# Optimization experiments

Hardware: AMD Instinct MI355X
Metric: run time of the kernel (lower is better)

Reference implementation:

```python
import jax, jax.numpy as jnp
import numpy as np

C = 64          # channels
L = 2           # GRU layers
DEC_STEPS = 35


def setup_inputs() -> dict:
    key = jax.random.key(0)
    ks = jax.random.split(key, 10)
    B, S = 2048, 512
    s = 0.1  # small init scale keeps gates in linear-ish region
    return {
        "pulse":    jax.random.normal(ks[0], (B, S, 2), dtype=jnp.float32),
        "dense1_w": jax.random.normal(ks[1], (C, 2), dtype=jnp.float32) * s,
        "dense1_b": jax.random.normal(ks[2], (C,), dtype=jnp.float32) * s,
        "dense2_w": jax.random.normal(ks[3], (2, C), dtype=jnp.float32) * s,
        "dense2_b": jax.random.normal(ks[4], (2,), dtype=jnp.float32) * s,
        "Wih":      jax.random.normal(ks[5], (L, 3 * C, C), dtype=jnp.float32) * s,
        "Whh":      jax.random.normal(ks[6], (L, 3 * C, C), dtype=jnp.float32) * s,
        "bih":      jax.random.normal(ks[7], (L, 3 * C), dtype=jnp.float32) * s,
        "bhh":      jax.random.normal(ks[8], (L, 3 * C), dtype=jnp.float32) * s,
        "embed":    jax.random.normal(ks[9], (1, C), dtype=jnp.float32) * s,
    }


def _gru_cell(x, h, wih, whh, bi, bh):
    # PyTorch GRU cell math (gate order r, z, n)
    gi = x @ wih.T + bi   # [B, 3C]
    gh = h @ whh.T + bh   # [B, 3C]
    ir, iz, inn = jnp.split(gi, 3, axis=-1)
    hr, hz, hn = jnp.split(gh, 3, axis=-1)
    r = jax.nn.sigmoid(ir + hr)
    z = jax.nn.sigmoid(iz + hz)
    n = jnp.tanh(inn + r * hn)
    return (1.0 - z) * n + z * h


def _multi_step(h_stack, x, Wih, Whh, bih, bhh):
    # One timestep through L stacked GRU layers. h_stack: [L, B, C]
    new_h = []
    inp = x
    for l in range(L):
        hl = _gru_cell(inp, h_stack[l], Wih[l], Whh[l], bih[l], bhh[l])
        new_h.append(hl)
        inp = hl
    return jnp.stack(new_h), inp  # (new state stack, top-layer output)


def reference(pulse, dense1_w, dense1_b, dense2_w, dense2_b, Wih, Whh, bih, bhh, embed):
    B = pulse.shape[0]
    # dense1 then time-major [S, B, C]
    x = pulse @ dense1_w.T + dense1_b
    x = jnp.transpose(x, (1, 0, 2))
    h0 = jnp.zeros((L, B, C), dtype=x.dtype)

    def enc_step(h, xt):
        h2, _ = _multi_step(h, xt, Wih, Whh, bih, bhh)
        return h2, None

    hT, _ = jax.lax.scan(enc_step, h0, x)  # encoder final state [L, B, C]

    sos = jnp.broadcast_to(embed[0], (B, C))  # embedding of token 0

    def dec_step(carry, _):
        latest, h = carry
        h2, out = _multi_step(h, latest, Wih, Whh, bih, bhh)
        return (out, h2), out

    _, outs = jax.lax.scan(dec_step, (sos, hT), None, length=DEC_STEPS)  # [35, B, C]

    # dense2 on decoder outputs; slicing pred[:, 1:, :] in the source drops the
    # sos position, which equals applying dense2 to the 35 decoder outputs only.
    pred = jnp.transpose(outs, (1, 0, 2)) @ dense2_w.T + dense2_b  # [B, 35, 2]
    return pred
```

## Files before the change

kernel.cpp:

```cpp
#include <hip/hip_runtime.h>
#include <math.h>


#define CCH  64
#define GG   192
#define SEQ  512
#define DECS 35
#define BT   8
#define NTH  512
#define NW   8
#define STG_SH (16 * 17 * 8)

typedef __attribute__((ext_vector_type(8))) short bf16x8;
typedef __attribute__((ext_vector_type(4))) float f32x4;

__device__ __forceinline__ short f2b(float f) {
  union { float f; unsigned u; } v; v.f = f;
  unsigned r = v.u + 0x7fffu + ((v.u >> 16) & 1u);
  return (short)(r >> 16);
}
__device__ __forceinline__ float sigf(float x) { return 1.0f / (1.0f + __expf(-x)); }
__device__ __forceinline__ float tanhfast(float x) {
  float t = __expf(-2.0f * fabsf(x));
  float r = (1.0f - t) / (1.0f + t);
  return copysignf(r, x);
}
__device__ __forceinline__ int stoff(int col, int k) {
  return ((k >> 3) * 17 + col) * 8 + (k & 7);
}

extern "C" __global__ void __launch_bounds__(NTH, 2)
gru_lane(const float* __restrict__ pulse,
         const float* __restrict__ d1w,
         const float* __restrict__ d1b,
         const float* __restrict__ d2w,
         const float* __restrict__ d2b,
         const float* __restrict__ Wih,
         const float* __restrict__ Whh,
         const float* __restrict__ bih,
         const float* __restrict__ bhh,
         const float* __restrict__ embed,
         float* __restrict__ out)
{
  __shared__ __align__(16) unsigned short stA[STG_SH];
  __shared__ __align__(16) unsigned short stC[STG_SH];
  __shared__ float red[NW * 16];

  const int tid = threadIdx.x;
  const int wid = tid >> 6;
  const int l   = tid & 63;
  const int lm  = l & 15;
  const int lg  = l >> 4;
  const int b   = lm & 7;
  const int ch  = wid * 8 + ((lm >> 3) << 2) + lg;
  const int bgb = blockIdx.x * BT;

  for (int i = tid; i < STG_SH; i += NTH) { stA[i] = 0; stC[i] = 0; }

  const float* Wih0 = Wih;
  const float* Whh0 = Whh;
  const float* Wih1 = Wih + GG * CCH;
  const float* Whh1 = Whh + GG * CCH;
  const int sub = lm & 3;
  bf16x8 bA[2][4], bC[2][4];
#pragma unroll
  for (int t = 0; t < 2; ++t) {
    const int wch = wid * 8 + t * 4 + (lm >> 2);
    const int rr  = (sub == 0 ? wch : (sub == 1 ? 64 + wch : 128 + wch));
#pragma unroll
    for (int s = 0; s < 4; ++s) {
#pragma unroll
      for (int e = 0; e < 8; ++e) {
        int kk = 32 * s + 8 * lg + e;
        float va, vc;
        if (sub == 2) {
          va = kk < 64 ? Wih0[rr * CCH + kk] : 0.f;
          vc = kk < 64 ? Wih1[rr * CCH + kk] : 0.f;
        } else if (sub == 3) {
          va = kk < 64 ? 0.f : Whh0[rr * CCH + kk - 64];
          vc = kk < 64 ? 0.f : Whh1[rr * CCH + kk - 64];
        } else {
          va = kk < 64 ? Wih0[rr * CCH + kk] : Whh0[rr * CCH + kk - 64];
          vc = kk < 64 ? Wih1[rr * CCH + kk] : Whh1[rr * CCH + kk - 64];
        }
        bA[t][s][e] = f2b(va);
        bC[t][s][e] = f2b(vc);
      }
    }
  }

  float A0f[3], A1f[3], C0f[3];
#pragma unroll
  for (int g = 0; g < 3; ++g) {
    int row = g * CCH + ch;
    float a0 = 0.f, a1 = 0.f, cc = 0.f;
    for (int k = 0; k < CCH; ++k) {
      float wv = Wih0[row * CCH + k];
      a0 += wv * d1w[2 * k];
      a1 += wv * d1w[2 * k + 1];
      cc += wv * d1b[k];
    }
    A0f[g] = a0; A1f[g] = a1; C0f[g] = cc + bih[row];
  }
  const float bh0r = bhh[ch], bh0z = bhh[64 + ch], bh0n = bhh[128 + ch];
  const float b0r = bih[ch] + bh0r, b0z = bih[64 + ch] + bh0z;
  const float bi0n = bih[128 + ch];
  const float b1r = bih[GG + ch] + bhh[GG + ch];
  const float b1z = bih[GG + 64 + ch] + bhh[GG + 64 + ch];
  const float bi1n = bih[GG + 128 + ch], bh1n = bhh[GG + 128 + ch];
  const float w2a = d2w[ch], w2b = d2w[CCH + ch];
  const float d2b0 = d2b[0], d2b1 = d2b[1];
  float h0 = 0.f, h1 = 0.f;
  short hb0 = 0, hb1 = 0;

  const float* prow = pulse + (size_t)(bgb + b) * SEQ * 2;
  __syncthreads();

  for (int t = 0; t < SEQ; ++t) {
    stC[stoff(b, 64 + ch)] = hb1;
    stC[stoff(8 + b, 64 + ch)] = hb1;
    float2 pv = *(const float2*)(prow + 2 * t);
    f32x4 a0 = {0.f, 0.f, 0.f, 0.f}, a1 = {0.f, 0.f, 0.f, 0.f};
#pragma unroll
    for (int s = 2; s < 4; ++s) {
      bf16x8 af = *(const bf16x8*)&stA[((s * 4 + lg) * 17 + lm) * 8];
      a0 = __builtin_amdgcn_mfma_f32_16x16x32_bf16(bA[0][s], af, a0, 0, 0, 0);
      a1 = __builtin_amdgcn_mfma_f32_16x16x32_bf16(bA[1][s], af, a1, 0, 0, 0);
    }
    {
      f32x4 g = (lm < 8) ? a0 : a1;
      float fr = pv.x * A0f[0] + pv.y * A1f[0] + C0f[0];
      float fz = pv.x * A0f[1] + pv.y * A1f[1] + C0f[1];
      float fn = pv.x * A0f[2] + pv.y * A1f[2] + C0f[2];
      float r = sigf(fr + g[0] + bh0r);
      float z = sigf(fz + g[1] + bh0z);
      float nn = tanhfast(fn + r * (g[3] + bh0n));
      h0 = (1.f - z) * nn + z * h0;
      hb0 = f2b(h0);
      stC[stoff(b, ch)] = hb0;
      stC[stoff(8 + b, ch)] = hb0;
    }
    __syncthreads();

    stA[stoff(b, 64 + ch)] = hb0;
    stA[stoff(8 + b, 64 + ch)] = hb0;
    f32x4 c0 = {0.f, 0.f, 0.f, 0.f}, c1 = {0.f, 0.f, 0.f, 0.f};
#pragma unroll
    for (int s = 0; s < 4; ++s) {
      bf16x8 cf = *(const bf16x8*)&stC[((s * 4 + lg) * 17 + lm) * 8];
      c0 = __builtin_amdgcn_mfma_f32_16x16x32_bf16(bC[0][s], cf, c0, 0, 0, 0);
      c1 = __builtin_amdgcn_mfma_f32_16x16x32_bf16(bC[1][s], cf, c1, 0, 0, 0);
    }
    {
      f32x4 g = (lm < 8) ? c0 : c1;
      float r = sigf(g[0] + b1r);
      float z = sigf(g[1] + b1z);
      float nn = tanhfast(g[2] + bi1n + r * (g[3] + bh1n));
      h1 = (1.f - z) * nn + z * h1;
      hb1 = f2b(h1);
    }
    __syncthreads();
  }

  {
    short eb = f2b(embed[ch]);
    stA[stoff(b, ch)] = eb;
    stA[stoff(8 + b, ch)] = eb;
  }
  __syncthreads();

  for (int d = 0; d < DECS; ++d) {
    stC[stoff(b, 64 + ch)] = hb1;
    stC[stoff(8 + b, 64 + ch)] = hb1;
    if (wid == 0 && l < 16 && d > 0) {
      int bb = l >> 1, o = l & 1;
      float s = 0.f;
#pragma unroll
      for (int w = 0; w < NW; ++w) s += red[w * 16 + bb * 2 + o];
      out[((size_t)(bgb + bb) * DECS + (d - 1)) * 2 + o] = s + (o ? d2b1 : d2b0);
    }
    f32x4 a0 = {0.f, 0.f, 0.f, 0.f}, a1 = {0.f, 0.f, 0.f, 0.f};
#pragma unroll
    for (int s = 0; s < 4; ++s) {
      bf16x8 af = *(const bf16x8*)&stA[((s * 4 + lg) * 17 + lm) * 8];
      a0 = __builtin_amdgcn_mfma_f32_16x16x32_bf16(bA[0][s], af, a0, 0, 0, 0);
      a1 = __builtin_amdgcn_mfma_f32_16x16x32_bf16(bA[1][s], af, a1, 0, 0, 0);
    }
    {
      f32x4 g = (lm < 8) ? a0 : a1;
      float r = sigf(g[0] + b0r);
      float z = sigf(g[1] + b0z);
      float nn = tanhfast(g[2] + bi0n + r * (g[3] + bh0n));
      h0 = (1.f - z) * nn + z * h0;
      hb0 = f2b(h0);
      stC[stoff(b, ch)] = hb0;
      stC[stoff(8 + b, ch)] = hb0;
    }
    __syncthreads();

    stA[stoff(b, 64 + ch)] = hb0;
    stA[stoff(8 + b, 64 + ch)] = hb0;
    f32x4 c0 = {0.f, 0.f, 0.f, 0.f}, c1 = {0.f, 0.f, 0.f, 0.f};
#pragma unroll
    for (int s = 0; s < 4; ++s) {
      bf16x8 cf = *(const bf16x8*)&stC[((s * 4 + lg) * 17 + lm) * 8];
      c0 = __builtin_amdgcn_mfma_f32_16x16x32_bf16(bC[0][s], cf, c0, 0, 0, 0);
      c1 = __builtin_amdgcn_mfma_f32_16x16x32_bf16(bC[1][s], cf, c1, 0, 0, 0);
    }
    {
      f32x4 g = (lm < 8) ? c0 : c1;
      float r = sigf(g[0] + b1r);
      float z = sigf(g[1] + b1z);
      float nn = tanhfast(g[2] + bi1n + r * (g[3] + bh1n));
      h1 = (1.f - z) * nn + z * h1;
      hb1 = f2b(h1);
      stA[stoff(b, ch)] = hb1;
      stA[stoff(8 + b, ch)] = hb1;
      float p0 = h1 * w2a, p1 = h1 * w2b;
      p0 += __shfl_xor(p0, 8);  p1 += __shfl_xor(p1, 8);
      p0 += __shfl_xor(p0, 16); p1 += __shfl_xor(p1, 16);
      p0 += __shfl_xor(p0, 32); p1 += __shfl_xor(p1, 32);
      if (l < 8) {
        red[wid * 16 + b * 2 + 0] = p0;
        red[wid * 16 + b * 2 + 1] = p1;
      }
    }
    __syncthreads();
  }

  if (wid == 0 && l < 16) {
    int bb = l >> 1, o = l & 1;
    float s = 0.f;
#pragma unroll
    for (int w = 0; w < NW; ++w) s += red[w * 16 + bb * 2 + o];
    out[((size_t)(bgb + bb) * DECS + (DECS - 1)) * 2 + o] = s + (o ? d2b1 : d2b0);
  }
}

extern "C" void kernel_launch(void* const* d_in, const int* in_sizes, int n_in,
                              void* d_out, int out_size, void* d_ws, size_t ws_size,
                              hipStream_t stream) {
  const float* pulse = (const float*)d_in[0];
  const float* d1w   = (const float*)d_in[1];
  const float* d1b   = (const float*)d_in[2];
  const float* d2w   = (const float*)d_in[3];
  const float* d2b   = (const float*)d_in[4];
  const float* Wih   = (const float*)d_in[5];
  const float* Whh   = (const float*)d_in[6];
  const float* bih   = (const float*)d_in[7];
  const float* bhh   = (const float*)d_in[8];
  const float* emb   = (const float*)d_in[9];
  float* out = (float*)d_out;

  int B = in_sizes[0] / (SEQ * 2);
  gru_lane<<<B / BT, NTH, 0, stream>>>(pulse, d1w, d1b, d2w, d2b,
                                       Wih, Whh, bih, bhh, emb, out);
}
```

Measured before the change: 577.0 us.

## Halve batch per block to four and double blocks per CU

Cuts each block's batch tile from 8 to 4 samples, giving twice as many blocks, and raises launch bounds to 4 blocks per SM. The lane-to-channel/batch mapping is remapped so each batch column is replicated into MFMA columns wc0/wc1, with the output reduction shuffles adjusted to match. The aim is more resident blocks to hide the latency of the serial recurrence. In exchange, half of each MFMA's columns carry duplicated data, so matrix work per sample doubles, and the tighter register budget may cause spills.

```diff
diff --git a/kernel.cpp b/kernel.cpp
--- a/kernel.cpp
+++ b/kernel.cpp
@@ -6,7 +6,7 @@
 #define GG   192
 #define SEQ  512
 #define DECS 35
-#define BT   8
+#define BT   4
 #define NTH  512
 #define NW   8
 #define STG_SH (16 * 17 * 8)
@@ -29,30 +29,34 @@
   return ((k >> 3) * 17 + col) * 8 + (k & 7);
 }
 
-extern "C" __global__ void __launch_bounds__(NTH, 2)
-gru_lane(const float* __restrict__ pulse,
-         const float* __restrict__ d1w,
-         const float* __restrict__ d1b,
-         const float* __restrict__ d2w,
-         const float* __restrict__ d2b,
-         const float* __restrict__ Wih,
-         const float* __restrict__ Whh,
-         const float* __restrict__ bih,
-         const float* __restrict__ bhh,
-         const float* __restrict__ embed,
-         float* __restrict__ out)
+extern "C" __global__ void __launch_bounds__(NTH, 4)
+gru_lane4(const float* __restrict__ pulse,
+          const float* __restrict__ d1w,
+          const float* __restrict__ d1b,
+          const float* __restrict__ d2w,
+          const float* __restrict__ d2b,
+          const float* __restrict__ Wih,
+          const float* __restrict__ Whh,
+          const float* __restrict__ bih,
+          const float* __restrict__ bhh,
+          const float* __restrict__ embed,
+          float* __restrict__ out)
 {
   __shared__ __align__(16) unsigned short stA[STG_SH];
   __shared__ __align__(16) unsigned short stC[STG_SH];
-  __shared__ float red[NW * 16];
+  __shared__ float red[NW * 8];
 
   const int tid = threadIdx.x;
   const int wid = tid >> 6;
   const int l   = tid & 63;
   const int lm  = l & 15;
   const int lg  = l >> 4;
-  const int b   = lm & 7;
-  const int ch  = wid * 8 + ((lm >> 3) << 2) + lg;
+  const int b   = lm & 3;
+  const int m   = lm >> 2;
+  const int tsel = m & 1;
+  const int ch  = wid * 8 + tsel * 4 + lg;
+  const int wc0 = b + (m >> 1) * 8;
+  const int wc1 = wc0 + 4;
   const int bgb = blockIdx.x * BT;
 
   for (int i = tid; i < STG_SH; i += NTH) { stA[i] = 0; stC[i] = 0; }
@@ -117,8 +121,8 @@
   __syncthreads();
 
   for (int t = 0; t < SEQ; ++t) {
-    stC[stoff(b, 64 + ch)] = hb1;
-    stC[stoff(8 + b, 64 + ch)] = hb1;
+    stC[stoff(wc0, 64 + ch)] = hb1;
+    stC[stoff(wc1, 64 + ch)] = hb1;
     float2 pv = *(const float2*)(prow + 2 * t);
     f32x4 a0 = {0.f, 0.f, 0.f, 0.f}, a1 = {0.f, 0.f, 0.f, 0.f};
 #pragma unroll
@@ -128,7 +132,7 @@
       a1 = __builtin_amdgcn_mfma_f32_16x16x32_bf16(bA[1][s], af, a1, 0, 0, 0);
     }
     {
-      f32x4 g = (lm < 8) ? a0 : a1;
+      f32x4 g = tsel ? a1 : a0;
       float fr = pv.x * A0f[0] + pv.y * A1f[0] + C0f[0];
       float fz = pv.x * A0f[1] + pv.y * A1f[1] + C0f[1];
       float fn = pv.x * A0f[2] + pv.y * A1f[2] + C0f[2];
@@ -137,13 +141,13 @@
       float nn = tanhfast(fn + r * (g[3] + bh0n));
       h0 = (1.f - z) * nn + z * h0;
       hb0 = f2b(h0);
-      stC[stoff(b, ch)] = hb0;
-      stC[stoff(8 + b, ch)] = hb0;
-    }
-    __syncthreads();
-
-    stA[stoff(b, 64 + ch)] = hb0;
-    stA[stoff(8 + b, 64 + ch)] = hb0;
+      stC[stoff(wc0, ch)] = hb0;
+      stC[stoff(wc1, ch)] = hb0;
+    }
+    __syncthreads();
+
+    stA[stoff(wc0, 64 + ch)] = hb0;
+    stA[stoff(wc1, 64 + ch)] = hb0;
     f32x4 c0 = {0.f, 0.f, 0.f, 0.f}, c1 = {0.f, 0.f, 0.f, 0.f};
 #pragma unroll
     for (int s = 0; s < 4; ++s) {
@@ -152,7 +156,7 @@
       c1 = __builtin_amdgcn_mfma_f32_16x16x32_bf16(bC[1][s], cf, c1, 0, 0, 0);
     }
     {
-      f32x4 g = (lm < 8) ? c0 : c1;
+      f32x4 g = tsel ? c1 : c0;
       float r = sigf(g[0] + b1r);
       float z = sigf(g[1] + b1z);
       float nn = tanhfast(g[2] + bi1n + r * (g[3] + bh1n));
@@ -164,19 +168,19 @@
 
   {
     short eb = f2b(embed[ch]);
-    stA[stoff(b, ch)] = eb;
-    stA[stoff(8 + b, ch)] = eb;
+    stA[stoff(wc0, ch)] = eb;
+    stA[stoff(wc1, ch)] = eb;
   }
   __syncthreads();
 
   for (int d = 0; d < DECS; ++d) {
-    stC[stoff(b, 64 + ch)] = hb1;
-    stC[stoff(8 + b, 64 + ch)] = hb1;
-    if (wid == 0 && l < 16 && d > 0) {
+    stC[stoff(wc0, 64 + ch)] = hb1;
+    stC[stoff(wc1, 64 + ch)] = hb1;
+    if (wid == 0 && l < 8 && d > 0) {
       int bb = l >> 1, o = l & 1;
       float s = 0.f;
 #pragma unroll
-      for (int w = 0; w < NW; ++w) s += red[w * 16 + bb * 2 + o];
+      for (int w = 0; w < NW; ++w) s += red[w * 8 + bb * 2 + o];
       out[((size_t)(bgb + bb) * DECS + (d - 1)) * 2 + o] = s + (o ? d2b1 : d2b0);
     }
     f32x4 a0 = {0.f, 0.f, 0.f, 0.f}, a1 = {0.f, 0.f, 0.f, 0.f};
@@ -187,19 +191,19 @@
       a1 = __builtin_amdgcn_mfma_f32_16x16x32_bf16(bA[1][s], af, a1, 0, 0, 0);
     }
     {
-      f32x4 g = (lm < 8) ? a0 : a1;
+      f32x4 g = tsel ? a1 : a0;
       float r = sigf(g[0] + b0r);
       float z = sigf(g[1] + b0z);
       float nn = tanhfast(g[2] + bi0n + r * (g[3] + bh0n));
       h0 = (1.f - z) * nn + z * h0;
       hb0 = f2b(h0);
-      stC[stoff(b, ch)] = hb0;
-      stC[stoff(8 + b, ch)] = hb0;
-    }
-    __syncthreads();
-
-    stA[stoff(b, 64 + ch)] = hb0;
-    stA[stoff(8 + b, 64 + ch)] = hb0;
+      stC[stoff(wc0, ch)] = hb0;
+      stC[stoff(wc1, ch)] = hb0;
+    }
+    __syncthreads();
+
+    stA[stoff(wc0, 64 + ch)] = hb0;
+    stA[stoff(wc1, 64 + ch)] = hb0;
     f32x4 c0 = {0.f, 0.f, 0.f, 0.f}, c1 = {0.f, 0.f, 0.f, 0.f};
 #pragma unroll
     for (int s = 0; s < 4; ++s) {
@@ -208,31 +212,31 @@
       c1 = __builtin_amdgcn_mfma_f32_16x16x32_bf16(bC[1][s], cf, c1, 0, 0, 0);
     }
     {
-      f32x4 g = (lm < 8) ? c0 : c1;
+      f32x4 g = tsel ? c1 : c0;
       float r = sigf(g[0] + b1r);
       float z = sigf(g[1] + b1z);
       float nn = tanhfast(g[2] + bi1n + r * (g[3] + bh1n));
       h1 = (1.f - z) * nn + z * h1;
       hb1 = f2b(h1);
-      stA[stoff(b, ch)] = hb1;
-      stA[stoff(8 + b, ch)] = hb1;
+      stA[stoff(wc0, ch)] = hb1;
+      stA[stoff(wc1, ch)] = hb1;
       float p0 = h1 * w2a, p1 = h1 * w2b;
-      p0 += __shfl_xor(p0, 8);  p1 += __shfl_xor(p1, 8);
+      p0 += __shfl_xor(p0, 4);  p1 += __shfl_xor(p1, 4);
       p0 += __shfl_xor(p0, 16); p1 += __shfl_xor(p1, 16);
       p0 += __shfl_xor(p0, 32); p1 += __shfl_xor(p1, 32);
-      if (l < 8) {
-        red[wid * 16 + b * 2 + 0] = p0;
-        red[wid * 16 + b * 2 + 1] = p1;
+      if (l < 4) {
+        red[wid * 8 + b * 2 + 0] = p0;
+        red[wid * 8 + b * 2 + 1] = p1;
       }
     }
     __syncthreads();
   }
 
-  if (wid == 0 && l < 16) {
+  if (wid == 0 && l < 8) {
     int bb = l >> 1, o = l & 1;
     float s = 0.f;
 #pragma unroll
-    for (int w = 0; w < NW; ++w) s += red[w * 16 + bb * 2 + o];
+    for (int w = 0; w < NW; ++w) s += red[w * 8 + bb * 2 + o];
     out[((size_t)(bgb + bb) * DECS + (DECS - 1)) * 2 + o] = s + (o ? d2b1 : d2b0);
   }
 }
@@ -253,6 +257,6 @@
   float* out = (float*)d_out;
 
   int B = in_sizes[0] / (SEQ * 2);
-  gru_lane<<<B / BT, NTH, 0, stream>>>(pulse, d1w, d1b, d2w, d2b,
-                                       Wih, Whh, bih, bhh, emb, out);
-}
+  gru_lane4<<<B / BT, NTH, 0, stream>>>(pulse, d1w, d1b, d2w, d2b,
+                                        Wih, Whh, bih, bhh, emb, out);
+}
```

After: 862.7 us. 49.5% more time.

## Pipeline GRU layers across warp groups with double-buffered LDS staging

Applied to the files above, without the earlier changes.

Splits the block into two warp groups: warps 0-3 compute layer 0 and warps 4-7 compute layer 1, one timestep behind, using ping-pong shared buffers. This needs one barrier per timestep instead of two, and the two layers run concurrently rather than in sequence. Each warp now handles four channel groups with 16 weight fragments, which raises register pressure. The pulse load for the next step is also prefetched. The decoder runs as an alternating two-phase schedule because its data dependence is serial.

```diff
diff --git a/kernel.cpp b/kernel.cpp
--- a/kernel.cpp
+++ b/kernel.cpp
@@ -8,7 +8,6 @@
 #define DECS 35
 #define BT   8
 #define NTH  512
-#define NW   8
 #define STG_SH (16 * 17 * 8)
 
 typedef __attribute__((ext_vector_type(8))) short bf16x8;
@@ -30,7 +29,7 @@
 }
 
 extern "C" __global__ void __launch_bounds__(NTH, 2)
-gru_lane(const float* __restrict__ pulse,
+gru_pipe(const float* __restrict__ pulse,
          const float* __restrict__ d1w,
          const float* __restrict__ d1b,
          const float* __restrict__ d2w,
@@ -42,198 +41,261 @@
          const float* __restrict__ embed,
          float* __restrict__ out)
 {
-  __shared__ __align__(16) unsigned short stA[STG_SH];
-  __shared__ __align__(16) unsigned short stC[STG_SH];
-  __shared__ float red[NW * 16];
-
-  const int tid = threadIdx.x;
-  const int wid = tid >> 6;
-  const int l   = tid & 63;
-  const int lm  = l & 15;
-  const int lg  = l >> 4;
-  const int b   = lm & 7;
-  const int ch  = wid * 8 + ((lm >> 3) << 2) + lg;
-  const int bgb = blockIdx.x * BT;
-
-  for (int i = tid; i < STG_SH; i += NTH) { stA[i] = 0; stC[i] = 0; }
-
-  const float* Wih0 = Wih;
-  const float* Whh0 = Whh;
-  const float* Wih1 = Wih + GG * CCH;
-  const float* Whh1 = Whh + GG * CCH;
+  __shared__ __align__(16) unsigned short stA[2][STG_SH];
+  __shared__ __align__(16) unsigned short stC[2][STG_SH];
+  __shared__ float red[4 * 8 * 2];
+
+  const int tid  = threadIdx.x;
+  const int wid  = tid >> 6;
+  const int l    = tid & 63;
+  const int role = wid >> 2;
+  const int wq   = wid & 3;
+  const int base = wq * 16;
+  const int lm   = l & 15;
+  const int lg   = l >> 4;
+  const int b    = lm & 7;
+  const int col  = lm;
+  const int bgb  = blockIdx.x * BT;
+
+  for (int i = tid; i < STG_SH; i += NTH) {
+    stA[0][i] = 0; stA[1][i] = 0; stC[0][i] = 0; stC[1][i] = 0;
+  }
+
+  const float* WihL = Wih + role * GG * CCH;
+  const float* WhhL = Whh + role * GG * CCH;
   const int sub = lm & 3;
-  bf16x8 bA[2][4], bC[2][4];
-#pragma unroll
-  for (int t = 0; t < 2; ++t) {
-    const int wch = wid * 8 + t * 4 + (lm >> 2);
+  bf16x8 bW[4][4];
+#pragma unroll
+  for (int t = 0; t < 4; ++t) {
+    const int wch = base + t * 4 + (lm >> 2);
     const int rr  = (sub == 0 ? wch : (sub == 1 ? 64 + wch : 128 + wch));
 #pragma unroll
     for (int s = 0; s < 4; ++s) {
 #pragma unroll
       for (int e = 0; e < 8; ++e) {
         int kk = 32 * s + 8 * lg + e;
-        float va, vc;
-        if (sub == 2) {
-          va = kk < 64 ? Wih0[rr * CCH + kk] : 0.f;
-          vc = kk < 64 ? Wih1[rr * CCH + kk] : 0.f;
-        } else if (sub == 3) {
-          va = kk < 64 ? 0.f : Whh0[rr * CCH + kk - 64];
-          vc = kk < 64 ? 0.f : Whh1[rr * CCH + kk - 64];
-        } else {
-          va = kk < 64 ? Wih0[rr * CCH + kk] : Whh0[rr * CCH + kk - 64];
-          vc = kk < 64 ? Wih1[rr * CCH + kk] : Whh1[rr * CCH + kk - 64];
+        float v;
+        if (sub == 2)      v = kk < 64 ? WihL[rr * CCH + kk] : 0.f;
+        else if (sub == 3) v = kk < 64 ? 0.f : WhhL[rr * CCH + kk - 64];
+        else               v = kk < 64 ? WihL[rr * CCH + kk]
+                                       : WhhL[rr * CCH + kk - 64];
+        bW[t][s][e] = f2b(v);
+      }
+    }
+  }
+
+  int chc[4];
+#pragma unroll
+  for (int t = 0; t < 4; ++t) chc[t] = base + t * 4 + lg;
+
+  float A0f[4][3], A1f[4][3], C0f[4][3];
+  float cR[4], cZ[4], ciN[4], chN[4];
+  float w2a[4], w2b[4];
+  if (!role) {
+#pragma unroll
+    for (int t = 0; t < 4; ++t) {
+      int ch = chc[t];
+#pragma unroll
+      for (int g = 0; g < 3; ++g) {
+        int row = g * CCH + ch;
+        float a0 = 0.f, a1 = 0.f, cc = 0.f;
+        for (int k = 0; k < CCH; ++k) {
+          float wv = Wih[row * CCH + k];
+          a0 += wv * d1w[2 * k];
+          a1 += wv * d1w[2 * k + 1];
+          cc += wv * d1b[k];
         }
-        bA[t][s][e] = f2b(va);
-        bC[t][s][e] = f2b(vc);
-      }
-    }
-  }
-
-  float A0f[3], A1f[3], C0f[3];
-#pragma unroll
-  for (int g = 0; g < 3; ++g) {
-    int row = g * CCH + ch;
-    float a0 = 0.f, a1 = 0.f, cc = 0.f;
-    for (int k = 0; k < CCH; ++k) {
-      float wv = Wih0[row * CCH + k];
-      a0 += wv * d1w[2 * k];
-      a1 += wv * d1w[2 * k + 1];
-      cc += wv * d1b[k];
-    }
-    A0f[g] = a0; A1f[g] = a1; C0f[g] = cc + bih[row];
-  }
-  const float bh0r = bhh[ch], bh0z = bhh[64 + ch], bh0n = bhh[128 + ch];
-  const float b0r = bih[ch] + bh0r, b0z = bih[64 + ch] + bh0z;
-  const float bi0n = bih[128 + ch];
-  const float b1r = bih[GG + ch] + bhh[GG + ch];
-  const float b1z = bih[GG + 64 + ch] + bhh[GG + 64 + ch];
-  const float bi1n = bih[GG + 128 + ch], bh1n = bhh[GG + 128 + ch];
-  const float w2a = d2w[ch], w2b = d2w[CCH + ch];
+        A0f[t][g] = a0; A1f[t][g] = a1; C0f[t][g] = cc + bih[row];
+      }
+      cR[t]  = bih[ch] + bhh[ch];
+      cZ[t]  = bih[64 + ch] + bhh[64 + ch];
+      ciN[t] = bih[128 + ch];
+      chN[t] = bhh[128 + ch];
+      w2a[t] = bhh[ch];
+      w2b[t] = bhh[64 + ch];
+    }
+  } else {
+#pragma unroll
+    for (int t = 0; t < 4; ++t) {
+      int ch = chc[t];
+      cR[t]  = bih[GG + ch] + bhh[GG + ch];
+      cZ[t]  = bih[GG + 64 + ch] + bhh[GG + 64 + ch];
+      ciN[t] = bih[GG + 128 + ch];
+      chN[t] = bhh[GG + 128 + ch];
+      w2a[t] = d2w[ch]; w2b[t] = d2w[CCH + ch];
+    }
+  }
   const float d2b0 = d2b[0], d2b1 = d2b[1];
-  float h0 = 0.f, h1 = 0.f;
-  short hb0 = 0, hb1 = 0;
+
+  if (!role) {
+#pragma unroll
+    for (int t = 0; t < 4; ++t) {
+      short eb = f2b(embed[chc[t]]);
+      stA[0][stoff(col, chc[t])] = eb;
+      stA[1][stoff(col, chc[t])] = eb;
+    }
+  }
+
+  float h[4] = {0.f, 0.f, 0.f, 0.f};
+  short hbv[4] = {0, 0, 0, 0};
+  __syncthreads();
+  int p = 0;
 
   const float* prow = pulse + (size_t)(bgb + b) * SEQ * 2;
-  __syncthreads();
-
+  float2 pv = role ? make_float2(0.f, 0.f) : *(const float2*)(prow);
   for (int t = 0; t < SEQ; ++t) {
-    stC[stoff(b, 64 + ch)] = hb1;
-    stC[stoff(8 + b, 64 + ch)] = hb1;
-    float2 pv = *(const float2*)(prow + 2 * t);
-    f32x4 a0 = {0.f, 0.f, 0.f, 0.f}, a1 = {0.f, 0.f, 0.f, 0.f};
-#pragma unroll
-    for (int s = 2; s < 4; ++s) {
-      bf16x8 af = *(const bf16x8*)&stA[((s * 4 + lg) * 17 + lm) * 8];
-      a0 = __builtin_amdgcn_mfma_f32_16x16x32_bf16(bA[0][s], af, a0, 0, 0, 0);
-      a1 = __builtin_amdgcn_mfma_f32_16x16x32_bf16(bA[1][s], af, a1, 0, 0, 0);
-    }
-    {
-      f32x4 g = (lm < 8) ? a0 : a1;
-      float fr = pv.x * A0f[0] + pv.y * A1f[0] + C0f[0];
-      float fz = pv.x * A0f[1] + pv.y * A1f[1] + C0f[1];
-      float fn = pv.x * A0f[2] + pv.y * A1f[2] + C0f[2];
-      float r = sigf(fr + g[0] + bh0r);
-      float z = sigf(fz + g[1] + bh0z);
-      float nn = tanhfast(fn + r * (g[3] + bh0n));
-      h0 = (1.f - z) * nn + z * h0;
-      hb0 = f2b(h0);
-      stC[stoff(b, ch)] = hb0;
-      stC[stoff(8 + b, ch)] = hb0;
+    if (!role) {
+      float2 pnx = pv;
+      if (t + 1 < SEQ) pnx = *(const float2*)(prow + 2 * (t + 1));
+      f32x4 acc[4] = {{0,0,0,0},{0,0,0,0},{0,0,0,0},{0,0,0,0}};
+#pragma unroll
+      for (int s = 2; s < 4; ++s) {
+        bf16x8 af = *(const bf16x8*)&stA[p][((s * 4 + lg) * 17 + lm) * 8];
+#pragma unroll
+        for (int q = 0; q < 4; ++q)
+          acc[q] = __builtin_amdgcn_mfma_f32_16x16x32_bf16(bW[q][s], af, acc[q], 0, 0, 0);
+      }
+#pragma unroll
+      for (int q = 0; q < 4; ++q) {
+        f32x4 g = acc[q];
+        float fr = pv.x * A0f[q][0] + pv.y * A1f[q][0] + C0f[q][0];
+        float fz = pv.x * A0f[q][1] + pv.y * A1f[q][1] + C0f[q][1];
+        float fn = pv.x * A0f[q][2] + pv.y * A1f[q][2] + C0f[q][2];
+        float r = sigf(fr + g[0] + w2a[q]);
+        float z = sigf(fz + g[1] + w2b[q]);
+        float nn = tanhfast(fn + r * (g[3] + chN[q]));
+        h[q] = (1.f - z) * nn + z * h[q];
+        hbv[q] = f2b(h[q]);
+        stA[p ^ 1][stoff(col, 64 + chc[q])] = hbv[q];
+        stC[p ^ 1][stoff(col, chc[q])]      = hbv[q];
+      }
+      pv = pnx;
+    } else if (t > 0) {
+      f32x4 acc[4] = {{0,0,0,0},{0,0,0,0},{0,0,0,0},{0,0,0,0}};
+#pragma unroll
+      for (int s = 0; s < 4; ++s) {
+        bf16x8 af = *(const bf16x8*)&stC[p][((s * 4 + lg) * 17 + lm) * 8];
+#pragma unroll
+        for (int q = 0; q < 4; ++q)
+          acc[q] = __builtin_amdgcn_mfma_f32_16x16x32_bf16(bW[q][s], af, acc[q], 0, 0, 0);
+      }
+#pragma unroll
+      for (int q = 0; q < 4; ++q) {
+        f32x4 g = acc[q];
+        float r = sigf(g[0] + cR[q]);
+        float z = sigf(g[1] + cZ[q]);
+        float nn = tanhfast(g[2] + ciN[q] + r * (g[3] + chN[q]));
+        h[q] = (1.f - z) * nn + z * h[q];
+        hbv[q] = f2b(h[q]);
+        stC[p ^ 1][stoff(col, 64 + chc[q])] = hbv[q];
+      }
     }
     __syncthreads();
-
-    stA[stoff(b, 64 + ch)] = hb0;
-    stA[stoff(8 + b, 64 + ch)] = hb0;
-    f32x4 c0 = {0.f, 0.f, 0.f, 0.f}, c1 = {0.f, 0.f, 0.f, 0.f};
+    p ^= 1;
+  }
+
+  {
+    f32x4 acc[4] = {{0,0,0,0},{0,0,0,0},{0,0,0,0},{0,0,0,0}};
+    const unsigned short* SB = role ? stC[p] : stA[p];
 #pragma unroll
     for (int s = 0; s < 4; ++s) {
-      bf16x8 cf = *(const bf16x8*)&stC[((s * 4 + lg) * 17 + lm) * 8];
-      c0 = __builtin_amdgcn_mfma_f32_16x16x32_bf16(bC[0][s], cf, c0, 0, 0, 0);
-      c1 = __builtin_amdgcn_mfma_f32_16x16x32_bf16(bC[1][s], cf, c1, 0, 0, 0);
-    }
-    {
-      f32x4 g = (lm < 8) ? c0 : c1;
-      float r = sigf(g[0] + b1r);
-      float z = sigf(g[1] + b1z);
-      float nn = tanhfast(g[2] + bi1n + r * (g[3] + bh1n));
-      h1 = (1.f - z) * nn + z * h1;
-      hb1 = f2b(h1);
+      bf16x8 af = *(const bf16x8*)&SB[((s * 4 + lg) * 17 + lm) * 8];
+#pragma unroll
+      for (int q = 0; q < 4; ++q)
+        acc[q] = __builtin_amdgcn_mfma_f32_16x16x32_bf16(bW[q][s], af, acc[q], 0, 0, 0);
+    }
+#pragma unroll
+    for (int q = 0; q < 4; ++q) {
+      f32x4 g = acc[q];
+      float r = sigf(g[0] + cR[q]);
+      float z = sigf(g[1] + cZ[q]);
+      float nn = tanhfast(g[2] + ciN[q] + r * (g[3] + chN[q]));
+      h[q] = (1.f - z) * nn + z * h[q];
+      hbv[q] = f2b(h[q]);
+      if (!role) {
+        stA[p ^ 1][stoff(col, 64 + chc[q])] = hbv[q];
+        stC[p ^ 1][stoff(col, chc[q])]      = hbv[q];
+      } else {
+        stC[p ^ 1][stoff(col, 64 + chc[q])] = hbv[q];
+      }
     }
     __syncthreads();
-  }
-
-  {
-    short eb = f2b(embed[ch]);
-    stA[stoff(b, ch)] = eb;
-    stA[stoff(8 + b, ch)] = eb;
-  }
-  __syncthreads();
+    p ^= 1;
+  }
 
   for (int d = 0; d < DECS; ++d) {
-    stC[stoff(b, 64 + ch)] = hb1;
-    stC[stoff(8 + b, 64 + ch)] = hb1;
-    if (wid == 0 && l < 16 && d > 0) {
-      int bb = l >> 1, o = l & 1;
-      float s = 0.f;
-#pragma unroll
-      for (int w = 0; w < NW; ++w) s += red[w * 16 + bb * 2 + o];
-      out[((size_t)(bgb + bb) * DECS + (d - 1)) * 2 + o] = s + (o ? d2b1 : d2b0);
-    }
-    f32x4 a0 = {0.f, 0.f, 0.f, 0.f}, a1 = {0.f, 0.f, 0.f, 0.f};
-#pragma unroll
-    for (int s = 0; s < 4; ++s) {
-      bf16x8 af = *(const bf16x8*)&stA[((s * 4 + lg) * 17 + lm) * 8];
-      a0 = __builtin_amdgcn_mfma_f32_16x16x32_bf16(bA[0][s], af, a0, 0, 0, 0);
-      a1 = __builtin_amdgcn_mfma_f32_16x16x32_bf16(bA[1][s], af, a1, 0, 0, 0);
-    }
-    {
-      f32x4 g = (lm < 8) ? a0 : a1;
-      float r = sigf(g[0] + b0r);
-      float z = sigf(g[1] + b0z);
-      float nn = tanhfast(g[2] + bi0n + r * (g[3] + bh0n));
-      h0 = (1.f - z) * nn + z * h0;
-      hb0 = f2b(h0);
-      stC[stoff(b, ch)] = hb0;
-      stC[stoff(8 + b, ch)] = hb0;
+    if (role) {
+      f32x4 acc[4] = {{0,0,0,0},{0,0,0,0},{0,0,0,0},{0,0,0,0}};
+#pragma unroll
+      for (int s = 0; s < 4; ++s) {
+        bf16x8 af = *(const bf16x8*)&stC[p][((s * 4 + lg) * 17 + lm) * 8];
+#pragma unroll
+        for (int q = 0; q < 4; ++q)
+          acc[q] = __builtin_amdgcn_mfma_f32_16x16x32_bf16(bW[q][s], af, acc[q], 0, 0, 0);
+      }
+      float p0 = 0.f, p1 = 0.f;
+#pragma unroll
+      for (int q = 0; q < 4; ++q) {
+        f32x4 g = acc[q];
+        float r = sigf(g[0] + cR[q]);
+        float z = sigf(g[1] + cZ[q]);
+        float nn = tanhfast(g[2] + ciN[q] + r * (g[3] + chN[q]));
+        h[q] = (1.f - z) * nn + z * h[q];
+        hbv[q] = f2b(h[q]);
+        stC[p ^ 1][stoff(col, 64 + chc[q])] = hbv[q];
+        stA[p ^ 1][stoff(col, chc[q])]      = hbv[q];
+        p0 += h[q] * w2a[q];
+        p1 += h[q] * w2b[q];
+      }
+      p0 += __shfl_xor(p0, 16); p0 += __shfl_xor(p0, 32);
+      p1 += __shfl_xor(p1, 16); p1 += __shfl_xor(p1, 32);
+      if (l < 8) {
+        red[((wid - 4) * 8 + b) * 2 + 0] = p0;
+        red[((wid - 4) * 8 + b) * 2 + 1] = p1;
+      }
+    } else {
+#pragma unroll
+      for (int q = 0; q < 4; ++q)
+        stA[p ^ 1][stoff(col, 64 + chc[q])] = hbv[q];
     }
     __syncthreads();
-
-    stA[stoff(b, 64 + ch)] = hb0;
-    stA[stoff(8 + b, 64 + ch)] = hb0;
-    f32x4 c0 = {0.f, 0.f, 0.f, 0.f}, c1 = {0.f, 0.f, 0.f, 0.f};
-#pragma unroll
-    for (int s = 0; s < 4; ++s) {
-      bf16x8 cf = *(const bf16x8*)&stC[((s * 4 + lg) * 17 + lm) * 8];
-      c0 = __builtin_amdgcn_mfma_f32_16x16x32_bf16(bC[0][s], cf, c0, 0, 0, 0);
-      c1 = __builtin_amdgcn_mfma_f32_16x16x32_bf16(bC[1][s], cf, c1, 0, 0, 0);
-    }
-    {
-      f32x4 g = (lm < 8) ? c0 : c1;
-      float r = sigf(g[0] + b1r);
-      float z = sigf(g[1] + b1z);
-      float nn = tanhfast(g[2] + bi1n + r * (g[3] + bh1n));
-      h1 = (1.f - z) * nn + z * h1;
-      hb1 = f2b(h1);
-      stA[stoff(b, ch)] = hb1;
-      stA[stoff(8 + b, ch)] = hb1;
-      float p0 = h1 * w2a, p1 = h1 * w2b;
-      p0 += __shfl_xor(p0, 8);  p1 += __shfl_xor(p1, 8);
-      p0 += __shfl_xor(p0, 16); p1 += __shfl_xor(p1, 16);
-      p0 += __shfl_xor(p0, 32); p1 += __shfl_xor(p1, 32);
-      if (l < 8) {
-        red[wid * 16 + b * 2 + 0] = p0;
-        red[wid * 16 + b * 2 + 1] = p1;
+    p ^= 1;
+
+    if (!role) {
+      if (d < DECS - 1) {
+        f32x4 acc[4] = {{0,0,0,0},{0,0,0,0},{0,0,0,0},{0,0,0,0}};
+#pragma unroll
+        for (int s = 0; s < 4; ++s) {
+          bf16x8 af = *(const bf16x8*)&stA[p][((s * 4 + lg) * 17 + lm) * 8];
+#pragma unroll
+          for (int q = 0; q < 4; ++q)
+            acc[q] = __builtin_amdgcn_mfma_f32_16x16x32_bf16(bW[q][s], af, acc[q], 0, 0, 0);
+        }
+#pragma unroll
+        for (int q = 0; q < 4; ++q) {
+          f32x4 g = acc[q];
+          float r = sigf(g[0] + cR[q]);
+          float z = sigf(g[1] + cZ[q]);
+          float nn = tanhfast(g[2] + ciN[q] + r * (g[3] + chN[q]));
+          h[q] = (1.f - z) * nn + z * h[q];
+          hbv[q] = f2b(h[q]);
+          stA[p ^ 1][stoff(col, 64 + chc[q])] = hbv[q];
+          stC[p ^ 1][stoff(col, chc[q])]      = hbv[q];
+        }
+      }
+    } else {
+#pragma unroll
+      for (int q = 0; q < 4; ++q)
+        stC[p ^ 1][stoff(col, 64 + chc[q])] = hbv[q];
+      if (wid == 4 && l < 16) {
+        int bb = l >> 1, o = l & 1;
+        float s_ = red[(0 * 8 + bb) * 2 + o] + red[(1 * 8 + bb) * 2 + o]
+                 + red[(2 * 8 + bb) * 2 + o] + red[(3 * 8 + bb) * 2 + o];
+        out[((size_t)(bgb + bb) * DECS + d) * 2 + o] = s_ + (o ? d2b1 : d2b0);
       }
     }
     __syncthreads();
-  }
-
-  if (wid == 0 && l < 16) {
-    int bb = l >> 1, o = l & 1;
-    float s = 0.f;
-#pragma unroll
-    for (int w = 0; w < NW; ++w) s += red[w * 16 + bb * 2 + o];
-    out[((size_t)(bgb + bb) * DECS + (DECS - 1)) * 2 + o] = s + (o ? d2b1 : d2b0);
+    p ^= 1;
   }
 }
 
@@ -253,6 +315,6 @@
   float* out = (float*)d_out;
 
   int B = in_sizes[0] / (SEQ * 2);
-  gru_lane<<<B / BT, NTH, 0, stream>>>(pulse, d1w, d1b, d2w, d2b,
+  gru_pipe<<<B / BT, NTH, 0, stream>>>(pulse, d1w, d1b, d2w, d2b,
                                        Wih, Whh, bih, bhh, emb, out);
 }
```

After: 769.1 us. 1.33x slower.
